# Performance work log

Hardware: AMD Instinct MI355X
Metric: run time of the kernel (lower is better)

The kernel has to match this reference:

```python
import jax, jax.numpy as jnp
import numpy as np

W_P, H_P = 2, 2  # patch rows, patch cols (size_of_patches[0])
HID, FC = 256, 1024

def _lstm_scan(x_seq, k, r, b):
    """Keras-style LSTM. x_seq: [T, N, Din] -> hidden states [T, N, H]."""
    N = x_seq.shape[1]
    H = r.shape[0]
    h0 = jnp.zeros((N, H), x_seq.dtype)
    c0 = jnp.zeros((N, H), x_seq.dtype)
    def step(carry, x):
        h, c = carry
        z = x @ k + h @ r + b  # [N, 4H], gate order i,f,g,o (keras)
        i, f, g, o = jnp.split(z, 4, axis=-1)
        c = jax.nn.sigmoid(f) * c + jax.nn.sigmoid(i) * jnp.tanh(g)
        h = jax.nn.sigmoid(o) * jnp.tanh(c)
        return (h, c), h
    _, hs = jax.lax.scan(step, (h0, c0), x_seq)
    return hs

def _bidir(x, k_f, r_f, b_f, k_b, r_b, b_b):
    # x: [T, N, D] -> [T, N, 2H]
    hf = _lstm_scan(x, k_f, r_f, b_f)
    hb = _lstm_scan(x[::-1], k_b, r_b, b_b)[::-1]
    return jnp.concatenate([hf, hb], axis=-1)

def reference(x, k_ud, r_ud, b_ud, k_du, r_du, b_du,
              k_lr, r_lr, b_lr, k_rl, r_rl, b_rl, Wd, bd):
    B, Hi, Wi, C = x.shape
    I, J = Hi // W_P, Wi // H_P
    # extract non-overlapping patches -> [B, I, J, w_p*h_p*C]
    p = x.reshape(B, I, W_P, J, H_P, C).transpose(0, 1, 3, 2, 4, 5)
    p = p.reshape(B, I, J, W_P * H_P * C)
    # vertical bidirectional sweep: sequence over rows i, batched over (B, J)
    v = p.transpose(1, 0, 2, 3).reshape(I, B * J, -1)          # [I, B*J, D]
    v = _bidir(v, k_ud, r_ud, b_ud, k_du, r_du, b_du)          # [I, B*J, 2H]
    v = v.reshape(I, B, J, -1).transpose(1, 0, 2, 3)           # [B, I, J, 2H]
    # horizontal bidirectional sweep: sequence over cols j, batched over (B, I)
    h = v.transpose(2, 0, 1, 3).reshape(J, B * I, -1)          # [J, B*I, 2H]
    h = _bidir(h, k_lr, r_lr, b_lr, k_rl, r_rl, b_rl)          # [J, B*I, 2H]
    h = h.reshape(J, B, I, -1).transpose(1, 2, 0, 3)           # [B, I, J, 2H]
    return jax.nn.relu(h @ Wd + bd)                            # [B, I, J, FC]

def setup_inputs() -> dict:
    key = jax.random.key(0)
    ks = jax.random.split(key, 16)
    D = W_P * H_P * 3
    def n(k, shape):
        return jax.random.normal(k, shape, dtype=jnp.float32) * 0.05
    inp = {"x": jax.random.normal(ks[0], (64, 64, 64, 3), dtype=jnp.float32)}
    for idx, (name, din) in enumerate([("ud", D), ("du", D), ("lr", 2 * HID), ("rl", 2 * HID)]):
        inp[f"k_{name}"] = n(ks[1 + 3 * idx], (din, 4 * HID))
        inp[f"r_{name}"] = n(ks[2 + 3 * idx], (HID, 4 * HID))
        inp[f"b_{name}"] = jnp.zeros((4 * HID,), jnp.float32)
    inp["Wd"] = n(ks[13], (2 * HID, FC))
    inp["bd"] = jnp.zeros((FC,), jnp.float32)
    return inp
```

## Files before the change

### kernel.cpp

```cpp
#include <hip/hip_runtime.h>
#include <math.h>
#include <stddef.h>
#include <stdint.h>


namespace {

typedef __bf16 bf16x8 __attribute__((ext_vector_type(8)));
typedef float f32x4 __attribute__((ext_vector_type(4)));
typedef __attribute__((address_space(1))) unsigned int as1_uint;
typedef __attribute__((address_space(3))) unsigned int as3_uint;

__device__ __forceinline__ float bf2f(ushort u) {
  return __builtin_bit_cast(float, (unsigned int)u << 16);
}
__device__ __forceinline__ ushort f2bf(float f) {
  unsigned int u = __builtin_bit_cast(unsigned int, f);
  u += 0x7fffu + ((u >> 16) & 1u);
  return (ushort)(u >> 16);
}
__device__ __forceinline__ unsigned int packbf(float a, float b) {
  return (unsigned int)f2bf(a) | ((unsigned int)f2bf(b) << 16);
}
__device__ __forceinline__ float sigm(float x) {
  return __fdividef(1.f, 1.f + __expf(-x));
}
__device__ __forceinline__ float tanh_(float x) {
  return 2.f * sigm(2.f * x) - 1.f;
}
__device__ __forceinline__ f32x4 mfma16(bf16x8 a, bf16x8 b, f32x4 c) {
  return __builtin_amdgcn_mfma_f32_16x16x32_bf16(a, b, c, 0, 0, 0);
}
__device__ __forceinline__ void load_lds16(const void* g, void* l) {
  __builtin_amdgcn_global_load_lds((const as1_uint*)g, (as3_uint*)l, 16, 0, 0);
}


__global__ __launch_bounds__(256) void transpose_all(
    const float* __restrict__ s0, const float* __restrict__ s1,
    const float* __restrict__ s2, ushort* __restrict__ d0,
    ushort* __restrict__ d1, ushort* __restrict__ d2) {
  const int which = blockIdx.y;
  const float* in = (which == 0) ? s0 : (which == 1) ? s1 : s2;
  ushort* out = (which == 0) ? d0 : (which == 1) ? d1 : d2;
  const int idx = blockIdx.x * 256 + threadIdx.x;
  const int n = idx >> 9, k = idx & 511;
  out[idx] = f2bf(in[k * 1024 + n]);
}

__global__ __launch_bounds__(256) void rfrag_all(
    const float* __restrict__ r0, const float* __restrict__ r1,
    const float* __restrict__ r2, const float* __restrict__ r3,
    ushort* __restrict__ out) {
  const int which = blockIdx.y;
  const float* r = (which == 0) ? r0 : (which == 1) ? r1 : (which == 2) ? r2 : r3;
  ushort* o = out + (size_t)which * 262144;
  const int id = blockIdx.x * 256 + threadIdx.x;
  const int lane = id & 63, kc = (id >> 6) & 7, tile = id >> 9;
  const int kbase = (kc << 5) + ((lane >> 4) << 3);
  const int col = (tile << 4) + (lane & 15);
  ushort tmp[8];
#pragma unroll
  for (int j = 0; j < 8; ++j) tmp[j] = f2bf(r[(size_t)(kbase + j) * 1024 + col]);
  *(uint4*)&o[(size_t)id << 3] = *(const uint4*)tmp;
}

__global__ __launch_bounds__(256) void zxv3_kernel(
    const float* __restrict__ x, const float* __restrict__ k0_,
    const float* __restrict__ b0_, const float* __restrict__ k1_,
    const float* __restrict__ b1_, uint4* __restrict__ Zf) {
  const int tid = threadIdx.x;
  const int jp = blockIdx.x, b = blockIdx.y, dir = blockIdx.z;
  const int j0 = jp << 1;
  const float* kw_ = dir ? k1_ : k0_;
  const float* bw_ = dir ? b1_ : b0_;
  __shared__ float ps[2][32][12];
  for (int e = tid; e < 2 * 32 * 12; e += 256) {
    const int jj = e / 384, rest = e - jj * 384;
    const int i = rest / 12, qq = rest - i * 12;
    const int pr = qq / 6, rem = qq - pr * 6;
    ps[jj][i][qq] =
        x[((size_t)((b * 64 + i * 2 + pr) * 64) + (j0 + jj) * 2 + rem / 3) * 3 + rem % 3];
  }
  __syncthreads();
  float kr[12][4], br[4];
#pragma unroll
  for (int qq = 0; qq < 12; ++qq)
#pragma unroll
    for (int g = 0; g < 4; ++g) kr[qq][g] = kw_[qq * 1024 + (g << 8) + tid];
#pragma unroll
  for (int g = 0; g < 4; ++g) br[g] = bw_[(g << 8) + tid];

  const int wv = tid >> 5, qv = (tid >> 4) & 1, l16v = tid & 15;
  const int rb16 = (b << 1) + (jp >> 3);
  const int n2l = jp & 7;
  const int kgz = n2l >> 1, pz = n2l & 1;
  const int tidz = (wv << 6) + (kgz << 4) + l16v;
  uint4* base = Zf + ((size_t)dir * 128 + rb16) * 65536;

  for (int i = 0; i < 32; ++i) {
    float z0[4], z1[4];
#pragma unroll
    for (int g = 0; g < 4; ++g) { z0[g] = br[g]; z1[g] = br[g]; }
#pragma unroll
    for (int qq = 0; qq < 12; ++qq) {
      const float p0 = ps[0][i][qq], p1 = ps[1][i][qq];
#pragma unroll
      for (int g = 0; g < 4; ++g) {
        z0[g] += p0 * kr[qq][g];
        z1[g] += p1 * kr[qq][g];
      }
    }
    uint4 o;
    o.x = packbf(z0[0], z1[0]);
    o.y = packbf(z0[1], z1[1]);
    o.z = packbf(z0[2], z1[2]);
    o.w = packbf(z0[3], z1[3]);
    base[(size_t)((((i << 1) + qv) << 1) + pz) * 512 + tidz] = o;
  }
}

__global__ __launch_bounds__(512) void lstm_sweep7(
    const uint4* __restrict__ Zf, const uint4* __restrict__ rF,
    ushort* __restrict__ outbuf, int vert) {
  const int tid = threadIdx.x;
  const int lane = tid & 63, w = tid >> 6;
  const int l16 = lane & 15, kg = lane >> 4;
  const int rb = blockIdx.x, dir = (int)blockIdx.y;
  const int rowbase = rb << 4;

  __shared__ ushort hbuf[2][16 * 256];

  const uint4* rFd = rF + (size_t)dir * 32768;
  const uint4* zb = Zf + ((size_t)dir * 128 + rb) * 65536;

  float cst[2][4];
#pragma unroll
  for (int q = 0; q < 2; ++q)
#pragma unroll
    for (int r = 0; r < 4; ++r) cst[q][r] = 0.f;

  uint4 zA[2], zB[2];
  {
    const int seq0 = dir ? 31 : 0;
    zA[0] = zb[(size_t)(seq0 << 2) * 512 + tid];
    zA[1] = zb[(size_t)((seq0 << 2) + 1) * 512 + tid];
  }

  for (int t = 0; t < 32; ++t) {
    const ushort* hprev = hbuf[(t + 1) & 1];
    ushort* hnext = hbuf[t & 1];

    if (t) {
      const int seqP = dir ? (32 - t) : (t - 1);
      const int row = tid >> 5, c4 = tid & 31;
      const uint4 v = *(const uint4*)((const char*)hprev + row * 512 +
                                      ((c4 ^ (row & 7)) << 4));
      const int n = rowbase + row, b = n >> 5, sp = n & 31;
      const int X = vert ? seqP : sp, Y = vert ? sp : seqP;
      *(uint4*)&outbuf[(((size_t)(b * 32 + X) * 32 + Y) << 9) + (dir << 8) +
                       (c4 << 3)] = v;
    }

#pragma unroll
    for (int q = 0; q < 2; ++q) {
      uint4(&zc)[2] = (q == 0) ? zA : zB;
      uint4(&zn)[2] = (q == 0) ? zB : zA;

      f32x4 acc[4];
#pragma unroll
      for (int g = 0; g < 4; ++g) {
        const unsigned int u0 = (g == 0) ? zc[0].x : (g == 1) ? zc[0].y
                                : (g == 2) ? zc[0].z : zc[0].w;
        const unsigned int u1 = (g == 0) ? zc[1].x : (g == 1) ? zc[1].y
                                : (g == 2) ? zc[1].z : zc[1].w;
        acc[g][0] = bf2f((ushort)(u0 & 0xffffu));
        acc[g][1] = bf2f((ushort)(u0 >> 16));
        acc[g][2] = bf2f((ushort)(u1 & 0xffffu));
        acc[g][3] = bf2f((ushort)(u1 >> 16));
      }

      if (t) {
        uint4 bfr[2][4];
#pragma unroll
        for (int g = 0; g < 4; ++g)
          bfr[0][g] = rFd[(size_t)(((g << 4) + (w << 1) + q) << 3) * 64 + lane];
#pragma unroll
        for (int kc = 0; kc < 8; ++kc) {
          const int cur = kc & 1;
          if (kc < 7) {
#pragma unroll
            for (int g = 0; g < 4; ++g)
              bfr[cur ^ 1][g] =
                  rFd[((size_t)(((g << 4) + (w << 1) + q) << 3) + kc + 1) * 64 +
                      lane];
          }
          const int c4 = (kc << 2) + kg;
          const uint4 a = *(const uint4*)((const char*)hprev + l16 * 512 +
                                          ((c4 ^ (l16 & 7)) << 4));
          const bf16x8 ab = __builtin_bit_cast(bf16x8, a);
#pragma unroll
          for (int g = 0; g < 4; ++g)
            acc[g] = mfma16(ab, __builtin_bit_cast(bf16x8, bfr[cur][g]), acc[g]);
        }
      }

      if (t < 31 || q == 0) {
        const int tn = q ? (t + 1) : t;
        const int qn = q ^ 1;
        const int seqn = dir ? (31 - tn) : tn;
        zn[0] = zb[(size_t)(((seqn << 1) + qn) << 1) * 512 + tid];
        zn[1] = zb[(size_t)((((seqn << 1) + qn) << 1) + 1) * 512 + tid];
      }

      const int col = (w << 5) + (q << 4) + l16;
#pragma unroll
      for (int r = 0; r < 4; ++r) {
        const float zi = acc[0][r];
        const float zf = acc[1][r];
        const float zg = acc[2][r];
        const float zo = acc[3][r];
        const float cn = sigm(zf) * cst[q][r] + sigm(zi) * tanh_(zg);
        cst[q][r] = cn;
        const float hv = sigm(zo) * tanh_(cn);
        const int row = (kg << 2) + r;
        *(ushort*)((char*)hnext + row * 512 +
                   (((col >> 3) ^ (row & 7)) << 4) + ((col & 7) << 1)) =
            f2bf(hv);
      }
    }
    __syncthreads();
  }

  {
    const int seqP = dir ? 0 : 31;
    const ushort* hl = hbuf[1];
    const int row = tid >> 5, c4 = tid & 31;
    const uint4 v = *(const uint4*)((const char*)hl + row * 512 +
                                    ((c4 ^ (row & 7)) << 4));
    const int n = rowbase + row, b = n >> 5, sp = n & 31;
    const int X = vert ? seqP : sp, Y = vert ? sp : seqP;
    *(uint4*)&outbuf[(((size_t)(b * 32 + X) * 32 + Y) << 9) + (dir << 8) +
                     (c4 << 3)] = v;
  }
}

__global__ __launch_bounds__(512) void gemm_bt_dual(
    const ushort* __restrict__ A, const ushort* __restrict__ BT0,
    const ushort* __restrict__ BT1, const float* __restrict__ bias0,
    const float* __restrict__ bias1, uint4* __restrict__ Zf) {
  const int tid = threadIdx.x;
  const int lane = tid & 63, wid = tid >> 6;
  const int l16 = lane & 15, kg = lane >> 4;
  const int wr = wid >> 1, wc = wid & 1;
  const int bid = blockIdx.x;
  const int xcd = bid & 7, lid = bid >> 3;
  const int m0 = ((xcd << 6) + (lid >> 4)) << 7;
  const int nb = lid & 15;
  const int dirq = nb >> 3;
  const int hc0 = (nb & 7) << 5;
  const ushort* BT = dirq ? BT1 : BT0;
  const float* bias = dirq ? bias1 : bias0;
  uint4* Cz = Zf + (size_t)dirq * 8388608;

  union SM {
    struct { uint4 A[128][8]; uint4 B[128][8]; } k;
    ushort eh[128][136];
  };
  __shared__ SM sm;

  f32x4 acc[2][4];
#pragma unroll
  for (int mt = 0; mt < 2; ++mt)
#pragma unroll
    for (int nt = 0; nt < 4; ++nt) acc[mt][nt] = (f32x4){0.f, 0.f, 0.f, 0.f};

  for (int k0 = 0; k0 < 512; k0 += 64) {
#pragma unroll
    for (int c = 0; c < 2; ++c) {
      const int cid = (wid << 7) + (c << 6) + lane;
      const int row = cid >> 3, ch = cid & 7;
      const int sch = ch ^ (row & 7);
      const int brow = ((row >> 5) << 8) + hc0 + (row & 31);
      load_lds16(A + (size_t)(m0 + row) * 512 + k0 + (sch << 3),
                 (uint4*)sm.k.A + (cid - lane));
      load_lds16(BT + (size_t)brow * 512 + k0 + (sch << 3),
                 (uint4*)sm.k.B + (cid - lane));
    }
    __syncthreads();
#pragma unroll
    for (int kk = 0; kk < 2; ++kk) {
      const int q = (kk << 2) + kg;
      bf16x8 a[2], b[4];
#pragma unroll
      for (int mt = 0; mt < 2; ++mt) {
        const int rr = (wr << 5) + (mt << 4) + l16;
        a[mt] = __builtin_bit_cast(bf16x8, sm.k.A[rr][q ^ (rr & 7)]);
      }
#pragma unroll
      for (int nt = 0; nt < 4; ++nt) {
        const int rr = (wc << 6) + (nt << 4) + l16;
        b[nt] = __builtin_bit_cast(bf16x8, sm.k.B[rr][q ^ (rr & 7)]);
      }
#pragma unroll
      for (int mt = 0; mt < 2; ++mt)
#pragma unroll
        for (int nt = 0; nt < 4; ++nt)
          acc[mt][nt] = mfma16(a[mt], b[nt], acc[mt][nt]);
    }
    __syncthreads();
  }

  float bn[4];
#pragma unroll
  for (int nt = 0; nt < 4; ++nt) {
    const int lcol = (wc << 6) + (nt << 4) + l16;
    bn[nt] = bias[((lcol >> 5) << 8) + hc0 + (lcol & 31)];
  }

#pragma unroll
  for (int mt = 0; mt < 2; ++mt) {
#pragma unroll
    for (int nt = 0; nt < 4; ++nt) {
      const int col = (wc << 6) + (nt << 4) + l16;
#pragma unroll
      for (int r = 0; r < 4; ++r) {
        const int rowl = (wr << 5) + (mt << 4) + (kg << 2) + r;
        sm.eh[rowl][col] = f2bf(acc[mt][nt][r] + bn[nt]);
      }
    }
  }
  __syncthreads();

#pragma unroll
  for (int h = 0; h < 2; ++h) {
    const int n_a = ((m0 >> 6) + h) << 1;
    const int rbz = n_a >> 4;
    const int n2l = (n_a & 15) >> 1;
    const int kgz = n2l >> 1, pz = n2l & 1;
#pragma unroll
    for (int it = 0; it < 2; ++it) {
      const int e = tid + (it << 9);
      const int seq = e >> 5, hl = e & 31;
      const int qv = hl >> 4, l16v = hl & 15;
      const int wz = (hc0 + hl) >> 5;
      const int tidz = (wz << 6) + (kgz << 4) + l16v;
      uint4 o;
      o.x = (unsigned int)sm.eh[(h << 6) + seq][hl] |
            ((unsigned int)sm.eh[(h << 6) + 32 + seq][hl] << 16);
      o.y = (unsigned int)sm.eh[(h << 6) + seq][32 + hl] |
            ((unsigned int)sm.eh[(h << 6) + 32 + seq][32 + hl] << 16);
      o.z = (unsigned int)sm.eh[(h << 6) + seq][64 + hl] |
            ((unsigned int)sm.eh[(h << 6) + 32 + seq][64 + hl] << 16);
      o.w = (unsigned int)sm.eh[(h << 6) + seq][96 + hl] |
            ((unsigned int)sm.eh[(h << 6) + 32 + seq][96 + hl] << 16);
      Cz[(size_t)rbz * 65536 + (size_t)((((seq << 1) + qv) << 1) + pz) * 512 +
         tidz] = o;
    }
  }
}

__global__ __launch_bounds__(512) void gemm_dense(
    const ushort* __restrict__ A, const ushort* __restrict__ BT,
    const float* __restrict__ bias, float* __restrict__ out) {
  const int tid = threadIdx.x;
  const int lane = tid & 63, wid = tid >> 6;
  const int l16 = lane & 15, kg = lane >> 4;
  const int wr = wid >> 1, wc = wid & 1;
  const int bid = blockIdx.x;
  const int xcd = bid & 7, lid = bid >> 3;
  const int m0 = ((xcd << 6) + (lid >> 3)) << 7;
  const int n0 = (lid & 7) << 7;

  union SM {
    struct { uint4 A[128][8]; uint4 B[128][8]; } k;
    float ef[64][132];
  };
  __shared__ SM sm;

  f32x4 acc[2][4];
#pragma unroll
  for (int mt = 0; mt < 2; ++mt)
#pragma unroll
    for (int nt = 0; nt < 4; ++nt) acc[mt][nt] = (f32x4){0.f, 0.f, 0.f, 0.f};

  for (int k0 = 0; k0 < 512; k0 += 64) {
#pragma unroll
    for (int c = 0; c < 2; ++c) {
      const int cid = (wid << 7) + (c << 6) + lane;
      const int row = cid >> 3, ch = cid & 7;
      const int sch = ch ^ (row & 7);
      load_lds16(A + (size_t)(m0 + row) * 512 + k0 + (sch << 3),
                 (uint4*)sm.k.A + (cid - lane));
      load_lds16(BT + (size_t)(n0 + row) * 512 + k0 + (sch << 3),
                 (uint4*)sm.k.B + (cid - lane));
    }
    __syncthreads();
#pragma unroll
    for (int kk = 0; kk < 2; ++kk) {
      const int q = (kk << 2) + kg;
      bf16x8 a[2], b[4];
#pragma unroll
      for (int mt = 0; mt < 2; ++mt) {
        const int rr = (wr << 5) + (mt << 4) + l16;
        a[mt] = __builtin_bit_cast(bf16x8, sm.k.A[rr][q ^ (rr & 7)]);
      }
#pragma unroll
      for (int nt = 0; nt < 4; ++nt) {
        const int rr = (wc << 6) + (nt << 4) + l16;
        b[nt] = __builtin_bit_cast(bf16x8, sm.k.B[rr][q ^ (rr & 7)]);
      }
#pragma unroll
      for (int mt = 0; mt < 2; ++mt)
#pragma unroll
        for (int nt = 0; nt < 4; ++nt)
          acc[mt][nt] = mfma16(a[mt], b[nt], acc[mt][nt]);
    }
    __syncthreads();
  }

  float bn[4];
#pragma unroll
  for (int nt = 0; nt < 4; ++nt)
    bn[nt] = bias[n0 + (wc << 6) + (nt << 4) + l16];

#pragma unroll
  for (int h = 0; h < 2; ++h) {
    __syncthreads();
    if ((wr >> 1) == h) {
#pragma unroll
      for (int mt = 0; mt < 2; ++mt) {
#pragma unroll
        for (int nt = 0; nt < 4; ++nt) {
          const int col = (wc << 6) + (nt << 4) + l16;
#pragma unroll
          for (int r = 0; r < 4; ++r) {
            const int rowl = ((wr & 1) << 5) + (mt << 4) + (kg << 2) + r;
            sm.ef[rowl][col] = fmaxf(acc[mt][nt][r] + bn[nt], 0.f);
          }
        }
      }
    }
    __syncthreads();
#pragma unroll
    for (int it = 0; it < 4; ++it) {
      const int c = tid + (it << 9);
      const int row = c >> 5, co = (c & 31) << 2;
      const f32x4 v = *(const f32x4*)&sm.ef[row][co];
      __builtin_nontemporal_store(
          v, (f32x4*)(out + (size_t)(m0 + (h << 6) + row) * 1024 + n0 + co));
    }
  }
}

}

extern "C" void kernel_launch(void* const* d_in, const int* in_sizes, int n_in,
                              void* d_out, int out_size, void* d_ws, size_t ws_size,
                              hipStream_t stream) {
  (void)in_sizes; (void)n_in; (void)out_size; (void)ws_size;
  const float* x    = (const float*)d_in[0];
  const float* k_ud = (const float*)d_in[1];
  const float* r_ud = (const float*)d_in[2];
  const float* b_ud = (const float*)d_in[3];
  const float* k_du = (const float*)d_in[4];
  const float* r_du = (const float*)d_in[5];
  const float* b_du = (const float*)d_in[6];
  const float* k_lr = (const float*)d_in[7];
  const float* r_lr = (const float*)d_in[8];
  const float* b_lr = (const float*)d_in[9];
  const float* k_rl = (const float*)d_in[10];
  const float* r_rl = (const float*)d_in[11];
  const float* b_rl = (const float*)d_in[12];
  const float* Wd   = (const float*)d_in[13];
  const float* bd   = (const float*)d_in[14];

  ushort* W    = (ushort*)d_ws;
  ushort* Z    = W;
  ushort* vbuf = Z + 134217728;
  ushort* rF   = vbuf + 33554432;
  ushort* kTh  = rF + 1048576;
  ushort* WdT  = kTh + 1048576;
  uint4* Zf = (uint4*)Z;

  rfrag_all<<<dim3(128, 4), 256, 0, stream>>>(r_ud, r_du, r_lr, r_rl, rF);
  transpose_all<<<dim3(2048, 3), 256, 0, stream>>>(k_lr, k_rl, Wd, kTh,
                                                   kTh + 524288, WdT);

  zxv3_kernel<<<dim3(16, 64, 2), 256, 0, stream>>>(x, k_ud, b_ud, k_du, b_du,
                                                   Zf);

  lstm_sweep7<<<dim3(128, 2), 512, 0, stream>>>(Zf, (const uint4*)rF, vbuf, 1);

  gemm_bt_dual<<<8192, 512, 0, stream>>>(vbuf, kTh, kTh + 524288, b_lr, b_rl,
                                         Zf);

  lstm_sweep7<<<dim3(128, 2), 512, 0, stream>>>(
      Zf, (const uint4*)(rF + 524288), vbuf, 0);

  gemm_dense<<<4096, 512, 0, stream>>>(vbuf, WdT, bd, (float*)d_out);
}
```

Baseline: 799.3 us.

## Stage recurrent weights through LDS double buffer and merge both column halves

The recurrent weight fragments are now streamed from global memory into a double-buffered shared-memory tile with async LDS loads, one k-chunk ahead. Each k-chunk load is then shared by both column halves, so the two half-steps are merged into one loop and every h fragment read feeds eight MFMAs. The change is meant to cut the redundant per-wave global loads of R and hide their latency behind the MFMAs. In exchange it uses 128KB of extra shared memory, adds a __syncthreads per k-chunk (eight per step), and prefetches all z inputs for the next step at once.

```diff
diff --git a/kernel.cpp b/kernel.cpp
--- a/kernel.cpp
+++ b/kernel.cpp
@@ -120,7 +120,7 @@
   }
 }
 
-__global__ __launch_bounds__(512) void lstm_sweep7(
+__global__ __launch_bounds__(512) void lstm_sweep12(
     const uint4* __restrict__ Zf, const uint4* __restrict__ rF,
     ushort* __restrict__ outbuf, int vert) {
   const int tid = threadIdx.x;
@@ -129,10 +129,12 @@
   const int rb = blockIdx.x, dir = (int)blockIdx.y;
   const int rowbase = rb << 4;
 
-  __shared__ ushort hbuf[2][16 * 256];
+  __shared__ uint4 rs[2][4096];
+  __shared__ ushort hbuf[2][4096];
 
   const uint4* rFd = rF + (size_t)dir * 32768;
   const uint4* zb = Zf + ((size_t)dir * 128 + rb) * 65536;
+  const int cb0 = tid - lane;
 
   float cst[2][4];
 #pragma unroll
@@ -140,11 +142,20 @@
 #pragma unroll
     for (int r = 0; r < 4; ++r) cst[q][r] = 0.f;
 
-  uint4 zA[2], zB[2];
+  uint4 zx[2][2];
   {
     const int seq0 = dir ? 31 : 0;
-    zA[0] = zb[(size_t)(seq0 << 2) * 512 + tid];
-    zA[1] = zb[(size_t)((seq0 << 2) + 1) * 512 + tid];
+#pragma unroll
+    for (int q = 0; q < 2; ++q)
+#pragma unroll
+      for (int p = 0; p < 2; ++p)
+        zx[q][p] = zb[(size_t)(((((seq0 << 1) + q) << 1) + p)) * 512 + tid];
+  }
+#pragma unroll
+  for (int i = 0; i < 8; ++i) {
+    const int T = w + (i << 3);
+    load_lds16(rFd + ((size_t)(T << 3)) * 64 + lane,
+               (uint4*)rs[0] + cb0 + (i << 9));
   }
 
   for (int t = 0; t < 32; ++t) {
@@ -153,73 +164,80 @@
 
     if (t) {
       const int seqP = dir ? (32 - t) : (t - 1);
-      const int row = tid >> 5, c4 = tid & 31;
+      const int row = tid >> 5, c4o = tid & 31;
       const uint4 v = *(const uint4*)((const char*)hprev + row * 512 +
-                                      ((c4 ^ (row & 7)) << 4));
+                                      ((c4o ^ (row & 7)) << 4));
       const int n = rowbase + row, b = n >> 5, sp = n & 31;
       const int X = vert ? seqP : sp, Y = vert ? sp : seqP;
       *(uint4*)&outbuf[(((size_t)(b * 32 + X) * 32 + Y) << 9) + (dir << 8) +
-                       (c4 << 3)] = v;
-    }
-
+                       (c4o << 3)] = v;
+    }
+
+    f32x4 acc[2][4];
 #pragma unroll
     for (int q = 0; q < 2; ++q) {
-      uint4(&zc)[2] = (q == 0) ? zA : zB;
-      uint4(&zn)[2] = (q == 0) ? zB : zA;
-
-      f32x4 acc[4];
 #pragma unroll
       for (int g = 0; g < 4; ++g) {
-        const unsigned int u0 = (g == 0) ? zc[0].x : (g == 1) ? zc[0].y
-                                : (g == 2) ? zc[0].z : zc[0].w;
-        const unsigned int u1 = (g == 0) ? zc[1].x : (g == 1) ? zc[1].y
-                                : (g == 2) ? zc[1].z : zc[1].w;
-        acc[g][0] = bf2f((ushort)(u0 & 0xffffu));
-        acc[g][1] = bf2f((ushort)(u0 >> 16));
-        acc[g][2] = bf2f((ushort)(u1 & 0xffffu));
-        acc[g][3] = bf2f((ushort)(u1 >> 16));
-      }
-
-      if (t) {
-        uint4 bfr[2][4];
-#pragma unroll
-        for (int g = 0; g < 4; ++g)
-          bfr[0][g] = rFd[(size_t)(((g << 4) + (w << 1) + q) << 3) * 64 + lane];
-#pragma unroll
-        for (int kc = 0; kc < 8; ++kc) {
-          const int cur = kc & 1;
-          if (kc < 7) {
-#pragma unroll
-            for (int g = 0; g < 4; ++g)
-              bfr[cur ^ 1][g] =
-                  rFd[((size_t)(((g << 4) + (w << 1) + q) << 3) + kc + 1) * 64 +
-                      lane];
+        const unsigned int u0 = (g == 0) ? zx[q][0].x : (g == 1) ? zx[q][0].y
+                                : (g == 2) ? zx[q][0].z : zx[q][0].w;
+        const unsigned int u1 = (g == 0) ? zx[q][1].x : (g == 1) ? zx[q][1].y
+                                : (g == 2) ? zx[q][1].z : zx[q][1].w;
+        acc[q][g][0] = bf2f((ushort)(u0 & 0xffffu));
+        acc[q][g][1] = bf2f((ushort)(u0 >> 16));
+        acc[q][g][2] = bf2f((ushort)(u1 & 0xffffu));
+        acc[q][g][3] = bf2f((ushort)(u1 >> 16));
+      }
+    }
+
+    if (t) {
+#pragma unroll
+      for (int kc = 0; kc < 8; ++kc) {
+        if (kc < 7 || t < 31) {
+          const int nk = (kc < 7) ? (kc + 1) : 0;
+          const int nbuf = (kc + 1) & 1;
+#pragma unroll
+          for (int i = 0; i < 8; ++i) {
+            const int T = w + (i << 3);
+            load_lds16(rFd + ((size_t)((T << 3) + nk)) * 64 + lane,
+                       (uint4*)rs[nbuf] + cb0 + (i << 9));
           }
-          const int c4 = (kc << 2) + kg;
-          const uint4 a = *(const uint4*)((const char*)hprev + l16 * 512 +
-                                          ((c4 ^ (l16 & 7)) << 4));
-          const bf16x8 ab = __builtin_bit_cast(bf16x8, a);
-#pragma unroll
-          for (int g = 0; g < 4; ++g)
-            acc[g] = mfma16(ab, __builtin_bit_cast(bf16x8, bfr[cur][g]), acc[g]);
         }
-      }
-
-      if (t < 31 || q == 0) {
-        const int tn = q ? (t + 1) : t;
-        const int qn = q ^ 1;
-        const int seqn = dir ? (31 - tn) : tn;
-        zn[0] = zb[(size_t)(((seqn << 1) + qn) << 1) * 512 + tid];
-        zn[1] = zb[(size_t)((((seqn << 1) + qn) << 1) + 1) * 512 + tid];
-      }
-
+        const int c4 = (kc << 2) + kg;
+        const uint4 a = *(const uint4*)((const char*)hprev + l16 * 512 +
+                                        ((c4 ^ (l16 & 7)) << 4));
+        const bf16x8 ab = __builtin_bit_cast(bf16x8, a);
+#pragma unroll
+        for (int q = 0; q < 2; ++q) {
+#pragma unroll
+          for (int g = 0; g < 4; ++g) {
+            const int T = (g << 4) + (w << 1) + q;
+            const bf16x8 bb =
+                __builtin_bit_cast(bf16x8, rs[kc & 1][(T << 6) + lane]);
+            acc[q][g] = mfma16(ab, bb, acc[q][g]);
+          }
+        }
+        __syncthreads();
+      }
+    }
+
+    if (t < 31) {
+      const int seqn = dir ? (30 - t) : (t + 1);
+#pragma unroll
+      for (int q = 0; q < 2; ++q)
+#pragma unroll
+        for (int p = 0; p < 2; ++p)
+          zx[q][p] = zb[(size_t)(((((seqn << 1) + q) << 1) + p)) * 512 + tid];
+    }
+
+#pragma unroll
+    for (int q = 0; q < 2; ++q) {
       const int col = (w << 5) + (q << 4) + l16;
 #pragma unroll
       for (int r = 0; r < 4; ++r) {
-        const float zi = acc[0][r];
-        const float zf = acc[1][r];
-        const float zg = acc[2][r];
-        const float zo = acc[3][r];
+        const float zi = acc[q][0][r];
+        const float zf = acc[q][1][r];
+        const float zg = acc[q][2][r];
+        const float zo = acc[q][3][r];
         const float cn = sigm(zf) * cst[q][r] + sigm(zi) * tanh_(zg);
         cst[q][r] = cn;
         const float hv = sigm(zo) * tanh_(cn);
@@ -235,13 +253,13 @@
   {
     const int seqP = dir ? 0 : 31;
     const ushort* hl = hbuf[1];
-    const int row = tid >> 5, c4 = tid & 31;
+    const int row = tid >> 5, c4o = tid & 31;
     const uint4 v = *(const uint4*)((const char*)hl + row * 512 +
-                                    ((c4 ^ (row & 7)) << 4));
+                                    ((c4o ^ (row & 7)) << 4));
     const int n = rowbase + row, b = n >> 5, sp = n & 31;
     const int X = vert ? seqP : sp, Y = vert ? sp : seqP;
     *(uint4*)&outbuf[(((size_t)(b * 32 + X) * 32 + Y) << 9) + (dir << 8) +
-                     (c4 << 3)] = v;
+                     (c4o << 3)] = v;
   }
 }
 
@@ -490,12 +508,13 @@
   zxv3_kernel<<<dim3(16, 64, 2), 256, 0, stream>>>(x, k_ud, b_ud, k_du, b_du,
                                                    Zf);
 
-  lstm_sweep7<<<dim3(128, 2), 512, 0, stream>>>(Zf, (const uint4*)rF, vbuf, 1);
+  lstm_sweep12<<<dim3(128, 2), 512, 0, stream>>>(Zf, (const uint4*)rF, vbuf,
+                                                 1);
 
   gemm_bt_dual<<<8192, 512, 0, stream>>>(vbuf, kTh, kTh + 524288, b_lr, b_rl,
                                          Zf);
 
-  lstm_sweep7<<<dim3(128, 2), 512, 0, stream>>>(
+  lstm_sweep12<<<dim3(128, 2), 512, 0, stream>>>(
       Zf, (const uint4*)(rF + 524288), vbuf, 0);
 
   gemm_dense<<<4096, 512, 0, stream>>>(vbuf, WdT, bd, (float*)d_out);
```

New measurement: 905.3 us. 13.3% more time.

## Fuse vertical input projection into the vertical LSTM sweep via MFMA

Applied to the files above, without the earlier changes.

Removes the separate zxv3 kernel, which wrote the vertical-sweep input projection Z to global memory. Now each LSTM step computes x·k + b in-kernel with one bf16 MFMA per gate tile, with the bias folded in as a constant-one input column. The projection weights are pre-packed into MFMA fragments by a small new kernel and staged in LDS, and the next step's patch pixels are prefetched from x. This drops a large global write and read of Z, at the cost of extra LDS use and MFMA work on the serial recurrence path.

```diff
diff --git a/kernel.cpp b/kernel.cpp
--- a/kernel.cpp
+++ b/kernel.cpp
@@ -65,58 +65,171 @@
   *(uint4*)&o[(size_t)id << 3] = *(const uint4*)tmp;
 }
 
-__global__ __launch_bounds__(256) void zxv3_kernel(
-    const float* __restrict__ x, const float* __restrict__ k0_,
-    const float* __restrict__ b0_, const float* __restrict__ k1_,
-    const float* __restrict__ b1_, uint4* __restrict__ Zf) {
+__global__ __launch_bounds__(256) void kfragv_kernel(
+    const float* __restrict__ k0, const float* __restrict__ b0,
+    const float* __restrict__ k1, const float* __restrict__ b1,
+    ushort* __restrict__ out) {
+  const int dir = blockIdx.y;
+  const int idx = blockIdx.x * 256 + threadIdx.x;
+  const int lane = idx & 63;
+  const int kbase = (lane >> 4) << 3;
+  const int col = ((idx >> 6) << 4) + (lane & 15);
+  const float* kw = dir ? k1 : k0;
+  const float* bw = dir ? b1 : b0;
+  ushort tmp[8];
+#pragma unroll
+  for (int j = 0; j < 8; ++j) {
+    const int kidx = kbase + j;
+    const float v = (kidx < 12) ? kw[kidx * 1024 + col]
+                  : (kidx == 12) ? bw[col] : 0.f;
+    tmp[j] = f2bf(v);
+  }
+  *(uint4*)&out[((size_t)dir * 4096 + idx) << 3] = *(const uint4*)tmp;
+}
+
+__global__ __launch_bounds__(512) void lstm_sweepV(
+    const float* __restrict__ x, const ushort* __restrict__ kfragV,
+    const uint4* __restrict__ rF, ushort* __restrict__ outbuf) {
   const int tid = threadIdx.x;
-  const int jp = blockIdx.x, b = blockIdx.y, dir = blockIdx.z;
-  const int j0 = jp << 1;
-  const float* kw_ = dir ? k1_ : k0_;
-  const float* bw_ = dir ? b1_ : b0_;
-  __shared__ float ps[2][32][12];
-  for (int e = tid; e < 2 * 32 * 12; e += 256) {
-    const int jj = e / 384, rest = e - jj * 384;
-    const int i = rest / 12, qq = rest - i * 12;
-    const int pr = qq / 6, rem = qq - pr * 6;
-    ps[jj][i][qq] =
-        x[((size_t)((b * 64 + i * 2 + pr) * 64) + (j0 + jj) * 2 + rem / 3) * 3 + rem % 3];
-  }
+  const int lane = tid & 63, w = tid >> 6;
+  const int l16 = lane & 15, kg = lane >> 4;
+  const int rb = blockIdx.x, dir = (int)blockIdx.y;
+  const int rowbase = rb << 4;
+  const int bb = rb >> 1;
+  const int jbase = (rb & 1) << 4;
+
+  __shared__ ushort hbuf[2][4096];
+  __shared__ uint4 kfr[4096];
+  __shared__ ushort pb[2][512];
+
+  const uint4* rFd = rF + (size_t)dir * 32768;
+
+  for (int e = tid; e < 640; e += 512) {
+    const int par = e / 320, rest = e - par * 320;
+    const int row = rest / 20, c = 12 + rest % 20;
+    pb[par][(row << 5) + c] = (c == 12) ? (ushort)0x3F80 : (ushort)0;
+  }
+  if (tid < 192) {
+    const int row = tid / 12, d = tid - row * 12;
+    const int pr = d / 6, rem = d - pr * 6, pc = rem / 3, c = rem - pc * 3;
+    const int i0 = dir ? 31 : 0;
+    const float v = x[((size_t)((bb * 64 + (i0 << 1) + pr) * 64) +
+                       ((jbase + row) << 1) + pc) * 3 + c];
+    pb[0][(row << 5) + d] = f2bf(v);
+  }
+#pragma unroll
+  for (int i = 0; i < 8; ++i)
+    load_lds16((const uint4*)kfragV + (size_t)dir * 4096 + tid + (i << 9),
+               kfr + (tid - lane) + (i << 9));
   __syncthreads();
-  float kr[12][4], br[4];
-#pragma unroll
-  for (int qq = 0; qq < 12; ++qq)
-#pragma unroll
-    for (int g = 0; g < 4; ++g) kr[qq][g] = kw_[qq * 1024 + (g << 8) + tid];
-#pragma unroll
-  for (int g = 0; g < 4; ++g) br[g] = bw_[(g << 8) + tid];
-
-  const int wv = tid >> 5, qv = (tid >> 4) & 1, l16v = tid & 15;
-  const int rb16 = (b << 1) + (jp >> 3);
-  const int n2l = jp & 7;
-  const int kgz = n2l >> 1, pz = n2l & 1;
-  const int tidz = (wv << 6) + (kgz << 4) + l16v;
-  uint4* base = Zf + ((size_t)dir * 128 + rb16) * 65536;
-
-  for (int i = 0; i < 32; ++i) {
-    float z0[4], z1[4];
-#pragma unroll
-    for (int g = 0; g < 4; ++g) { z0[g] = br[g]; z1[g] = br[g]; }
-#pragma unroll
-    for (int qq = 0; qq < 12; ++qq) {
-      const float p0 = ps[0][i][qq], p1 = ps[1][i][qq];
+
+  float cst[2][4];
+#pragma unroll
+  for (int q = 0; q < 2; ++q)
+#pragma unroll
+    for (int r = 0; r < 4; ++r) cst[q][r] = 0.f;
+
+  for (int t = 0; t < 32; ++t) {
+    const int seq = dir ? (31 - t) : t;
+    const ushort* hprev = hbuf[(t + 1) & 1];
+    ushort* hnext = hbuf[t & 1];
+
+    if (t) {
+      const int seqP = dir ? (32 - t) : (t - 1);
+      const int row = tid >> 5, c4o = tid & 31;
+      const uint4 v = *(const uint4*)((const char*)hprev + row * 512 +
+                                      ((c4o ^ (row & 7)) << 4));
+      const int n = rowbase + row, b = n >> 5, sp = n & 31;
+      *(uint4*)&outbuf[(((size_t)(b * 32 + seqP) * 32 + sp) << 9) +
+                       (dir << 8) + (c4o << 3)] = v;
+    }
+
+    float pv = 0.f;
+    if (t < 31 && tid < 192) {
+      const int row = tid / 12, d = tid - row * 12;
+      const int pr = d / 6, rem = d - pr * 6, pc = rem / 3, c = rem - pc * 3;
+      const int iN = dir ? (30 - t) : (t + 1);
+      pv = x[((size_t)((bb * 64 + (iN << 1) + pr) * 64) +
+              ((jbase + row) << 1) + pc) * 3 + c];
+    }
+
+    const bf16x8 pf = __builtin_bit_cast(
+        bf16x8, *(const uint4*)&pb[t & 1][(l16 << 5) + (kg << 3)]);
+    f32x4 acc[2][4];
+#pragma unroll
+    for (int q = 0; q < 2; ++q) {
 #pragma unroll
       for (int g = 0; g < 4; ++g) {
-        z0[g] += p0 * kr[qq][g];
-        z1[g] += p1 * kr[qq][g];
-      }
-    }
-    uint4 o;
-    o.x = packbf(z0[0], z1[0]);
-    o.y = packbf(z0[1], z1[1]);
-    o.z = packbf(z0[2], z1[2]);
-    o.w = packbf(z0[3], z1[3]);
-    base[(size_t)((((i << 1) + qv) << 1) + pz) * 512 + tidz] = o;
+        const int tile = (g << 4) + (w << 1) + q;
+        const bf16x8 kb = __builtin_bit_cast(bf16x8, kfr[(tile << 6) + lane]);
+        acc[q][g] = mfma16(pf, kb, (f32x4){0.f, 0.f, 0.f, 0.f});
+      }
+    }
+
+    if (t) {
+#pragma unroll
+      for (int q = 0; q < 2; ++q) {
+        uint4 bfr[2][4];
+#pragma unroll
+        for (int g = 0; g < 4; ++g)
+          bfr[0][g] = rFd[(size_t)(((g << 4) + (w << 1) + q) << 3) * 64 + lane];
+#pragma unroll
+        for (int kc = 0; kc < 8; ++kc) {
+          const int cur = kc & 1;
+          if (kc < 7) {
+#pragma unroll
+            for (int g = 0; g < 4; ++g)
+              bfr[cur ^ 1][g] =
+                  rFd[((size_t)(((g << 4) + (w << 1) + q) << 3) + kc + 1) * 64 +
+                      lane];
+          }
+          const int c4 = (kc << 2) + kg;
+          const uint4 a = *(const uint4*)((const char*)hprev + l16 * 512 +
+                                          ((c4 ^ (l16 & 7)) << 4));
+          const bf16x8 ab = __builtin_bit_cast(bf16x8, a);
+#pragma unroll
+          for (int g = 0; g < 4; ++g)
+            acc[q][g] =
+                mfma16(ab, __builtin_bit_cast(bf16x8, bfr[cur][g]), acc[q][g]);
+        }
+      }
+    }
+
+    if (t < 31 && tid < 192) {
+      const int row = tid / 12, d = tid - row * 12;
+      pb[(t + 1) & 1][(row << 5) + d] = f2bf(pv);
+    }
+
+#pragma unroll
+    for (int q = 0; q < 2; ++q) {
+      const int col = (w << 5) + (q << 4) + l16;
+#pragma unroll
+      for (int r = 0; r < 4; ++r) {
+        const float zi = acc[q][0][r];
+        const float zf = acc[q][1][r];
+        const float zg = acc[q][2][r];
+        const float zo = acc[q][3][r];
+        const float cn = sigm(zf) * cst[q][r] + sigm(zi) * tanh_(zg);
+        cst[q][r] = cn;
+        const float hv = sigm(zo) * tanh_(cn);
+        const int row = (kg << 2) + r;
+        *(ushort*)((char*)hnext + row * 512 +
+                   (((col >> 3) ^ (row & 7)) << 4) + ((col & 7) << 1)) =
+            f2bf(hv);
+      }
+    }
+    __syncthreads();
+  }
+
+  {
+    const int seqP = dir ? 0 : 31;
+    const ushort* hl = hbuf[1];
+    const int row = tid >> 5, c4o = tid & 31;
+    const uint4 v = *(const uint4*)((const char*)hl + row * 512 +
+                                    ((c4o ^ (row & 7)) << 4));
+    const int n = rowbase + row, b = n >> 5, sp = n & 31;
+    *(uint4*)&outbuf[(((size_t)(b * 32 + seqP) * 32 + sp) << 9) + (dir << 8) +
+                     (c4o << 3)] = v;
   }
 }
 
@@ -129,7 +242,7 @@
   const int rb = blockIdx.x, dir = (int)blockIdx.y;
   const int rowbase = rb << 4;
 
-  __shared__ ushort hbuf[2][16 * 256];
+  __shared__ ushort hbuf[2][4096];
 
   const uint4* rFd = rF + (size_t)dir * 32768;
   const uint4* zb = Zf + ((size_t)dir * 128 + rb) * 65536;
@@ -475,22 +588,23 @@
   const float* Wd   = (const float*)d_in[13];
   const float* bd   = (const float*)d_in[14];
 
-  ushort* W    = (ushort*)d_ws;
-  ushort* Z    = W;
-  ushort* vbuf = Z + 134217728;
-  ushort* rF   = vbuf + 33554432;
-  ushort* kTh  = rF + 1048576;
-  ushort* WdT  = kTh + 1048576;
+  ushort* W     = (ushort*)d_ws;
+  ushort* Z     = W;
+  ushort* vbuf  = Z + 134217728;
+  ushort* rF    = vbuf + 33554432;
+  ushort* kTh   = rF + 1048576;
+  ushort* WdT   = kTh + 1048576;
+  ushort* kfragV = WdT + 524288;
   uint4* Zf = (uint4*)Z;
 
   rfrag_all<<<dim3(128, 4), 256, 0, stream>>>(r_ud, r_du, r_lr, r_rl, rF);
   transpose_all<<<dim3(2048, 3), 256, 0, stream>>>(k_lr, k_rl, Wd, kTh,
                                                    kTh + 524288, WdT);
-
-  zxv3_kernel<<<dim3(16, 64, 2), 256, 0, stream>>>(x, k_ud, b_ud, k_du, b_du,
-                                                   Zf);
-
-  lstm_sweep7<<<dim3(128, 2), 512, 0, stream>>>(Zf, (const uint4*)rF, vbuf, 1);
+  kfragv_kernel<<<dim3(16, 2), 256, 0, stream>>>(k_ud, b_ud, k_du, b_du,
+                                                 kfragV);
+
+  lstm_sweepV<<<dim3(128, 2), 512, 0, stream>>>(x, kfragV, (const uint4*)rF,
+                                                vbuf);
 
   gemm_bt_dual<<<8192, 512, 0, stream>>>(vbuf, kTh, kTh + 524288, b_lr, b_rl,
                                          Zf);
```

Measured after the change: 716.4 us. 1.12x faster.
